# Optimization experiments

Measured on AMD Instinct MI355X. Metric: run time of the kernel, lower is better.

The kernel has to match this reference:

```python
import jax, jax.numpy as jnp
import numpy as np

B, C, D, H, W = 16, 4, 64, 64, 64


def setup_inputs() -> dict:
    key = jax.random.key(0)
    k1, k2 = jax.random.split(key)
    inp = jax.random.normal(k1, (B, C, D, H, W), dtype=jnp.float32)
    lab = jax.random.normal(k2, (B, C, D, H, W), dtype=jnp.float32)
    return {"input": inp, "label": lab}


def reference(input, label):
    b, c, d, h, w = input.shape
    n = d * h * w
    num_features = int(np.ceil(0.5 * n))  # static top-k size, ceil(0.5*D*H*W)
    # Flatten (batch, channel) pairs: [B*C, N]
    diff = (input - label).reshape(b * c, n)
    # Per-slice top-k of |diff|. Since mse over the selected indices equals
    # mean(|diff|_topk ** 2), we only need the top-k values.
    vals, _ = jax.lax.top_k(jnp.abs(diff), num_features)  # [B*C, k]
    per_slice_mse = jnp.mean(vals * vals, axis=-1)  # [B*C]
    loss = jnp.sum(per_slice_mse) / b
    return loss.reshape(1)
```

## Files before the change

### kernel.cpp

```cpp
#include <hip/hip_runtime.h>
#include <stdint.h>

#define NSLICE 64
#define N_ELEM 262144
#define K_TOP  131072
#define INV_KB (1.0f / (131072.0f * 16.0f))

#define NB     2048
#define SHIFT  20

#define SNCH    4
#define SSTRIDE (N_ELEM / SNCH)
#define RANK_A  2048
#define BLK    256

#define BLK_M  1024
#define CPB    4
#define CHUNK  (N_ELEM / CPB)

__device__ __forceinline__ unsigned int absbits(float d) {
    return __float_as_uint(d) & 0x7fffffffu;
}

__global__ __launch_bounds__(BLK) void k_thresh(const float* __restrict__ in,
                                                const float* __restrict__ lab,
                                                float* __restrict__ t2arr,
                                                float* __restrict__ sliceS,
                                                unsigned int* __restrict__ sliceC) {
    __shared__ unsigned int hc[NB];
    __shared__ unsigned int part[BLK];
    __shared__ unsigned int pref[BLK];
    const int tid = threadIdx.x;
    const int slice = blockIdx.x;
    for (int i = tid; i < NB; i += BLK) hc[i] = 0u;
    if (tid == 0) sliceS[slice] = 0.0f;
    if (tid == 1) sliceC[slice] = 0u;
    __syncthreads();
#pragma unroll
    for (int j = 0; j < SNCH; ++j) {
        const long base = (long)slice * N_ELEM + (long)j * SSTRIDE;
        const float4 a = ((const float4*)(in + base))[tid];
        const float4 b = ((const float4*)(lab + base))[tid];
        atomicAdd(&hc[absbits(a.x - b.x) >> SHIFT], 1u);
        atomicAdd(&hc[absbits(a.y - b.y) >> SHIFT], 1u);
        atomicAdd(&hc[absbits(a.z - b.z) >> SHIFT], 1u);
        atomicAdd(&hc[absbits(a.w - b.w) >> SHIFT], 1u);
    }
    __syncthreads();
    const int G = NB / BLK;
    unsigned int loc[NB / BLK];
    unsigned int s = 0;
#pragma unroll
    for (int j = 0; j < G; ++j) {
        loc[j] = hc[tid * G + j];
        s += loc[j];
    }
    part[tid] = s;
    __syncthreads();
    if (tid == 0) {
        unsigned int c = 0;
        for (int i = 0; i < BLK; ++i) { pref[i] = c; c += part[i]; }
    }
    __syncthreads();
    unsigned int cum = pref[tid];
#pragma unroll
    for (int j = 0; j < G; ++j) {
        const unsigned int c = loc[j];
        if (cum <= RANK_A && RANK_A < cum + c) {
            const unsigned int p = (unsigned int)(tid * G + j);
            const float f = (float)(RANK_A - cum) / (float)c;
            const unsigned int tbits = (p << SHIFT)
                                     + (unsigned int)(f * (float)(1u << SHIFT));
            const float t = __uint_as_float(tbits);
            t2arr[slice] = t * t;
        }
        cum += c;
    }
}

__global__ __launch_bounds__(BLK_M, 4) void k_main(const float* __restrict__ in,
                                                   const float* __restrict__ lab,
                                                   const float* __restrict__ t2arr,
                                                   float* __restrict__ sliceS,
                                                   unsigned int* __restrict__ sliceC) {
    const int tid = threadIdx.x;
    const int slice = blockIdx.y;
    const float t2 = t2arr[slice];
    const long base = (long)slice * N_ELEM + (long)blockIdx.x * CHUNK;
    const float4* a4 = (const float4*)(in + base);
    const float4* b4 = (const float4*)(lab + base);

    float S0 = 0.0f, S1 = 0.0f;
    unsigned int C0 = 0u, C1 = 0u;
#pragma unroll 4
    for (int i = tid; i < CHUNK / 4; i += BLK_M) {
        const float4 a = a4[i];
        const float4 b = b4[i];
        {
            float d = a.x - b.x; float sq = d * d; bool g = sq > t2;
            S0 += g ? sq : 0.0f; C0 += g ? 1u : 0u;
        }
        {
            float d = a.y - b.y; float sq = d * d; bool g = sq > t2;
            S1 += g ? sq : 0.0f; C1 += g ? 1u : 0u;
        }
        {
            float d = a.z - b.z; float sq = d * d; bool g = sq > t2;
            S0 += g ? sq : 0.0f; C0 += g ? 1u : 0u;
        }
        {
            float d = a.w - b.w; float sq = d * d; bool g = sq > t2;
            S1 += g ? sq : 0.0f; C1 += g ? 1u : 0u;
        }
    }
    float S = S0 + S1;
    unsigned int C = C0 + C1;
#pragma unroll
    for (int off = 32; off > 0; off >>= 1) {
        S += __shfl_down(S, off);
        C += __shfl_down(C, off);
    }
    if ((tid & 63) == 0) {
        atomicAdd(&sliceS[slice], S);
        atomicAdd(&sliceC[slice], C);
    }
}

__global__ __launch_bounds__(64) void k_final(const float* __restrict__ sliceS,
                                              const unsigned int* __restrict__ sliceC,
                                              const float* __restrict__ t2arr,
                                              float* __restrict__ out) {
    const int t = threadIdx.x;
    float S = sliceS[t] + ((float)K_TOP - (float)sliceC[t]) * t2arr[t];
#pragma unroll
    for (int off = 32; off > 0; off >>= 1) S += __shfl_down(S, off);
    if (t == 0) out[0] = S * INV_KB;
}

extern "C" void kernel_launch(void* const* d_in, const int* in_sizes, int n_in,
                              void* d_out, int out_size, void* d_ws, size_t ws_size,
                              hipStream_t stream) {
    const float* in = (const float*)d_in[0];
    const float* lab = (const float*)d_in[1];
    float* out = (float*)d_out;

    unsigned char* w = (unsigned char*)d_ws;
    float* t2arr = (float*)(w);
    float* sliceS = (float*)(w + 256);
    unsigned int* sliceC = (unsigned int*)(w + 512);

    k_thresh<<<NSLICE, BLK, 0, stream>>>(in, lab, t2arr, sliceS, sliceC);
    k_main<<<dim3(CPB, NSLICE), BLK_M, 0, stream>>>(in, lab, t2arr, sliceS, sliceC);
    k_final<<<1, 64, 0, stream>>>(sliceS, sliceC, t2arr, out);
}
```

Measured before the change: 47.93 us.

## Double-buffer loads in main reduction kernel with smaller blocks and more chunks

The main threshold-sum kernel now uses 256-thread blocks and splits each slice into 8 chunks instead of 4. Its strided loop is replaced by an explicit two-batch software pipeline in which each batch holds four float4 pairs per thread, so the next loads are issued while the current batch is consumed. The aim is to keep more memory requests in flight and hide global load latency in this bandwidth-bound pass. The cost is higher register use, since 16 float4 values are held per thread, which may limit occupancy, plus more blocks and more atomics per slice.

```diff
diff --git a/kernel.cpp b/kernel.cpp
--- a/kernel.cpp
+++ b/kernel.cpp
@@ -14,9 +14,10 @@
 #define RANK_A  2048
 #define BLK    256
 
-#define BLK_M  1024
-#define CPB    4
-#define CHUNK  (N_ELEM / CPB)
+#define BLK_M   256
+#define CPB     8
+#define CHUNK   (N_ELEM / CPB)
+#define NBATCH  8
 
 __device__ __forceinline__ unsigned int absbits(float d) {
     return __float_as_uint(d) & 0x7fffffffu;
@@ -78,6 +79,44 @@
     }
 }
 
+struct Batch {
+    float4 a[4];
+    float4 b[4];
+};
+
+__device__ __forceinline__ void loadB(Batch& p, const float4* __restrict__ a4,
+                                      const float4* __restrict__ b4, int off) {
+#pragma unroll
+    for (int j = 0; j < 4; ++j) {
+        p.a[j] = a4[off + j * BLK_M];
+        p.b[j] = b4[off + j * BLK_M];
+    }
+}
+
+__device__ __forceinline__ void consB(const Batch& p, float t2,
+                                      float& S0, float& S1,
+                                      unsigned int& C0, unsigned int& C1) {
+#pragma unroll
+    for (int j = 0; j < 4; ++j) {
+        {
+            float d = p.a[j].x - p.b[j].x; float sq = d * d; bool g = sq > t2;
+            S0 += g ? sq : 0.0f; C0 += g ? 1u : 0u;
+        }
+        {
+            float d = p.a[j].y - p.b[j].y; float sq = d * d; bool g = sq > t2;
+            S1 += g ? sq : 0.0f; C1 += g ? 1u : 0u;
+        }
+        {
+            float d = p.a[j].z - p.b[j].z; float sq = d * d; bool g = sq > t2;
+            S0 += g ? sq : 0.0f; C0 += g ? 1u : 0u;
+        }
+        {
+            float d = p.a[j].w - p.b[j].w; float sq = d * d; bool g = sq > t2;
+            S1 += g ? sq : 0.0f; C1 += g ? 1u : 0u;
+        }
+    }
+}
+
 __global__ __launch_bounds__(BLK_M, 4) void k_main(const float* __restrict__ in,
                                                    const float* __restrict__ lab,
                                                    const float* __restrict__ t2arr,
@@ -92,27 +131,18 @@
 
     float S0 = 0.0f, S1 = 0.0f;
     unsigned int C0 = 0u, C1 = 0u;
-#pragma unroll 4
-    for (int i = tid; i < CHUNK / 4; i += BLK_M) {
-        const float4 a = a4[i];
-        const float4 b = b4[i];
-        {
-            float d = a.x - b.x; float sq = d * d; bool g = sq > t2;
-            S0 += g ? sq : 0.0f; C0 += g ? 1u : 0u;
-        }
-        {
-            float d = a.y - b.y; float sq = d * d; bool g = sq > t2;
-            S1 += g ? sq : 0.0f; C1 += g ? 1u : 0u;
-        }
-        {
-            float d = a.z - b.z; float sq = d * d; bool g = sq > t2;
-            S0 += g ? sq : 0.0f; C0 += g ? 1u : 0u;
-        }
-        {
-            float d = a.w - b.w; float sq = d * d; bool g = sq > t2;
-            S1 += g ? sq : 0.0f; C1 += g ? 1u : 0u;
-        }
+
+    Batch X, Y;
+    loadB(X, a4, b4, tid);
+    loadB(Y, a4, b4, tid + 4 * BLK_M);
+#pragma unroll
+    for (int b = 0; b < NBATCH; b += 2) {
+        consB(X, t2, S0, S1, C0, C1);
+        if (b + 2 < NBATCH) loadB(X, a4, b4, tid + (b + 2) * 4 * BLK_M);
+        consB(Y, t2, S0, S1, C0, C1);
+        if (b + 3 < NBATCH) loadB(Y, a4, b4, tid + (b + 3) * 4 * BLK_M);
     }
+
     float S = S0 + S1;
     unsigned int C = C0 + C1;
 #pragma unroll
```

Result: faster. 40.50 us (-15.5%).

## Split main pass into smaller blocks with software-pipelined loads

Applied to the files above, without the earlier changes.

Shrinks k_main blocks from 1024 to 256 threads and raises chunks per slice from 4 to 32, so the grid has many more blocks and each thread handles exactly 8 float4 pairs. The loop is replaced by straight-line code that keeps up to four loads in flight ahead of the compute, with sched_barrier calls stopping the compiler from reordering them. The goal is more memory-level parallelism and better latency hiding on this bandwidth-bound pass. In exchange, more blocks perform per-wavefront atomics on the same slice counters, and the fully unrolled code raises register use.

```diff
diff --git a/kernel.cpp b/kernel.cpp
--- a/kernel.cpp
+++ b/kernel.cpp
@@ -14,9 +14,9 @@
 #define RANK_A  2048
 #define BLK    256
 
-#define BLK_M  1024
-#define CPB    4
-#define CHUNK  (N_ELEM / CPB)
+#define BLK_M   256
+#define CPB     32
+#define CHUNK   (N_ELEM / CPB)
 
 __device__ __forceinline__ unsigned int absbits(float d) {
     return __float_as_uint(d) & 0x7fffffffu;
@@ -78,6 +78,18 @@
     }
 }
 
+#define LOADP(j) { va##j = a4[tid + (j) * BLK_M]; vb##j = b4[tid + (j) * BLK_M]; }
+#define CONSP(j) { \
+    { float d = va##j.x - vb##j.x; float sq = d * d; bool g = sq > t2; \
+      S0 += g ? sq : 0.0f; C0 += g ? 1u : 0u; } \
+    { float d = va##j.y - vb##j.y; float sq = d * d; bool g = sq > t2; \
+      S1 += g ? sq : 0.0f; C1 += g ? 1u : 0u; } \
+    { float d = va##j.z - vb##j.z; float sq = d * d; bool g = sq > t2; \
+      S0 += g ? sq : 0.0f; C0 += g ? 1u : 0u; } \
+    { float d = va##j.w - vb##j.w; float sq = d * d; bool g = sq > t2; \
+      S1 += g ? sq : 0.0f; C1 += g ? 1u : 0u; } }
+#define SB __builtin_amdgcn_sched_barrier(0);
+
 __global__ __launch_bounds__(BLK_M, 4) void k_main(const float* __restrict__ in,
                                                    const float* __restrict__ lab,
                                                    const float* __restrict__ t2arr,
@@ -92,27 +104,18 @@
 
     float S0 = 0.0f, S1 = 0.0f;
     unsigned int C0 = 0u, C1 = 0u;
-#pragma unroll 4
-    for (int i = tid; i < CHUNK / 4; i += BLK_M) {
-        const float4 a = a4[i];
-        const float4 b = b4[i];
-        {
-            float d = a.x - b.x; float sq = d * d; bool g = sq > t2;
-            S0 += g ? sq : 0.0f; C0 += g ? 1u : 0u;
-        }
-        {
-            float d = a.y - b.y; float sq = d * d; bool g = sq > t2;
-            S1 += g ? sq : 0.0f; C1 += g ? 1u : 0u;
-        }
-        {
-            float d = a.z - b.z; float sq = d * d; bool g = sq > t2;
-            S0 += g ? sq : 0.0f; C0 += g ? 1u : 0u;
-        }
-        {
-            float d = a.w - b.w; float sq = d * d; bool g = sq > t2;
-            S1 += g ? sq : 0.0f; C1 += g ? 1u : 0u;
-        }
-    }
+
+    float4 va0, vb0, va1, vb1, va2, vb2, va3, vb3;
+    float4 va4, vb4, va5, vb5, va6, vb6, va7, vb7;
+
+    LOADP(0) LOADP(1) LOADP(2) SB
+    LOADP(3) SB CONSP(0)
+    LOADP(4) SB CONSP(1)
+    LOADP(5) SB CONSP(2)
+    LOADP(6) SB CONSP(3)
+    LOADP(7) SB CONSP(4)
+    CONSP(5) CONSP(6) CONSP(7)
+
     float S = S0 + S1;
     unsigned int C = C0 + C1;
 #pragma unroll
```

Measured after the change: 78.78 us. +64.4%, slower.
